# Kernel optimization log

Measured on AMD Instinct MI355X. Metric: run time of the kernel, lower is better.

The kernel has to match this reference:

```python
import jax, jax.numpy as jnp
import numpy as np

N, E, M = 100000, 1600000, 10000
D_IN, D_HID, D_OUT = 128, 128, 128


def setup_inputs() -> dict:
    key = jax.random.key(0)
    ks = jax.random.split(key, 16)
    feat = jax.random.normal(ks[0], (N, D_IN), dtype=jnp.float32)
    src = jax.random.randint(ks[1], (E,), 0, N, dtype=jnp.int32)
    dst = jax.random.randint(ks[2], (E,), 0, N, dtype=jnp.int32)
    masked_offset = jax.random.randint(ks[3], (M,), 0, N, dtype=jnp.int32)
    def xavier(k, shape):
        fan_in, fan_out = shape[0], shape[1]
        a = jnp.sqrt(6.0 / (fan_in + fan_out))
        return jax.random.uniform(k, shape, jnp.float32, -a, a)
    return {
        'feat': feat, 'src': src, 'dst': dst, 'masked_offset': masked_offset,
        # GraphConv layers (weight [in,out], bias [out])
        'W1': xavier(ks[4], (D_IN, D_HID)), 'b1': jnp.zeros((D_HID,), jnp.float32),
        'W2': xavier(ks[5], (D_HID, D_HID)), 'b2': jnp.zeros((D_HID,), jnp.float32),
        # fusion MLP
        'Wm1': xavier(ks[6], (D_HID + D_IN, D_HID)), 'bm1': jnp.zeros((D_HID,), jnp.float32),
        'Wm2': xavier(ks[7], (D_HID, D_HID)), 'bm2': jnp.zeros((D_HID,), jnp.float32),
        'Wm3': xavier(ks[8], (D_HID, D_OUT)),  # final Linear has bias=False
    }


def _graph_conv_right(h, src, dst, W, b, inv_deg):
    # DGL GraphConv(norm='right'): aggregate src features at dst, divide by in-degree.
    # Apply weight first (in_feats >= out_feats path) -- mathematically identical.
    hw = h @ W                                   # [N, out]
    agg = jax.ops.segment_sum(hw[src], dst, num_segments=N)  # scatter-add over edges
    return agg * inv_deg + b


def reference(feat, src, dst, masked_offset, W1, b1, W2, b2, Wm1, bm1, Wm2, bm2, Wm3):
    ones = jnp.ones((E,), jnp.float32)
    deg = jax.ops.segment_sum(ones, dst, num_segments=N)
    inv_deg = (1.0 / jnp.clip(deg, 1.0, None))[:, None]      # [N,1]
    # GCN layer 1 + ReLU (Identity norm)
    h = jax.nn.relu(_graph_conv_right(feat, src, dst, W1, b1, inv_deg))
    # GCN layer 2 (last layer: no activation; dropout no-op at eval)
    h = _graph_conv_right(h, src, dst, W2, b2, inv_deg)
    # fusion == 'cat': relu(Identity(h[masked])) concat raw features
    hm = jax.nn.relu(h[masked_offset])                       # [M, H]
    x = jnp.concatenate([hm, feat[masked_offset]], axis=1)   # [M, H+D]
    x = jax.nn.relu(x @ Wm1 + bm1)
    x = jax.nn.relu(x @ Wm2 + bm2)
    return x @ Wm3
```

## Files before the change

### kernel.cpp

```cpp
#include <hip/hip_runtime.h>

#define NN 100000
#define NE 1600000
#define NM 10000
#define NSB 256
#define SUBN 391
#define CAP2 7424
#define PCH 2048
#define NBP2 782
#define NBTB 1600
#define NBWC 48

typedef __attribute__((ext_vector_type(8))) short bf16x8;
typedef __attribute__((ext_vector_type(4))) float f32x4;

__device__ inline float4 ld4(const float* p) { return *(const float4*)p; }
__device__ inline float bf2f(unsigned short u) {
  union { unsigned int i; float f; } c; c.i = ((unsigned int)u) << 16; return c.f;
}
__device__ inline unsigned short f2bf(float f) {
  union { float f; unsigned int i; } c; c.f = f;
  unsigned int u = c.i + 0x7fffu + ((c.i >> 16) & 1u);
  return (unsigned short)(u >> 16);
}
__device__ inline void stx(unsigned char* base, int rowBytes, int row, int col,
                           unsigned short val) {
  int bc = col * 2;
  int c = bc >> 4, cp = c ^ (row & 15);
  *(unsigned short*)&base[row * rowBytes + (cp << 4) + (bc & 15)] = val;
}
__device__ inline bf16x8 ldx8(const unsigned char* base, int rowBytes, int row, int kc) {
  return *(const bf16x8*)&base[row * rowBytes + ((kc ^ (row & 15)) << 4)];
}

__device__ inline void convfrag(const float* W, unsigned short* Wf, int g) {
  int k8 = (g >> 7) << 3, col = g & 127;
  unsigned short tmp[8];
#pragma unroll
  for (int i = 0; i < 8; ++i) tmp[i] = f2bf(W[(k8 + i) * 128 + col]);
  *(uint4*)&Wf[(size_t)g * 8] = *(const uint4*)tmp;
}

__global__ __launch_bounds__(256) void front_k(const int* __restrict__ src,
                                               const int* __restrict__ dst,
                                               unsigned* __restrict__ parts2,
                                               int* __restrict__ pcnt2,
                                               const float* __restrict__ feat,
                                               unsigned short* __restrict__ featbf,
                                               const float* W1, const float* W2,
                                               const float* Wm1, const float* Wm2,
                                               const float* Wm3,
                                               unsigned short* W1f, unsigned short* W2f,
                                               unsigned short* Wm1f, unsigned short* Wm2f,
                                               unsigned short* Wm3f,
                                               unsigned short* __restrict__ h1bf) {
  __shared__ int cntw[4][NSB];
  __shared__ int basew[4][NSB];
  __shared__ int bstart[NSB + 1];
  __shared__ int gbase[NSB];
  __shared__ int wsum[4];
  __shared__ unsigned buf[PCH];
  __shared__ unsigned char bb[PCH];
  const int bid = blockIdx.x;
  const int tid = threadIdx.x;

  if (bid < NBP2) {
    const int wv = tid >> 6;
    const int e0 = bid * PCH;
    for (int i = tid; i < 4 * NSB; i += 256) ((int*)cntw)[i] = 0;
    __syncthreads();
    unsigned pk[8];
    int b_[8], lp_[8];
#pragma unroll
    for (int j = 0; j < 8; ++j) {
      int e = e0 + j * 256 + tid;
      bool ok = e < NE;
      int s = ok ? src[e] : 0;
      int d = ok ? dst[e] : 0;
      int b = d / SUBN;
      int ld = d - b * SUBN;
      pk[j] = ((unsigned)ld << 17) | (unsigned)s;
      b_[j] = ok ? b : -1;
      if (ok) lp_[j] = atomicAdd(&cntw[wv][b], 1);
    }
    __syncthreads();
    int t0 = cntw[0][tid], t1 = cntw[1][tid], t2 = cntw[2][tid], t3 = cntw[3][tid];
    int tot = t0 + t1 + t2 + t3;
    int x = tot;
#pragma unroll
    for (int d = 1; d < 64; d <<= 1) {
      int y = __shfl_up(x, d, 64);
      if ((tid & 63) >= d) x += y;
    }
    if ((tid & 63) == 63) wsum[wv] = x;
    __syncthreads();
    int woff = 0;
#pragma unroll
    for (int w = 0; w < 4; ++w) woff += (w < wv) ? wsum[w] : 0;
    int excl = x + woff - tot;
    bstart[tid] = excl;
    basew[0][tid] = excl;
    basew[1][tid] = excl + t0;
    basew[2][tid] = excl + t0 + t1;
    basew[3][tid] = excl + t0 + t1 + t2;
    gbase[tid] = atomicAdd(&pcnt2[tid], tot);
    if (tid == NSB - 1) bstart[NSB] = excl + tot;
    __syncthreads();
#pragma unroll
    for (int j = 0; j < 8; ++j)
      if (b_[j] >= 0) {
        int pos = basew[wv][b_[j]] + lp_[j];
        buf[pos] = pk[j];
        bb[pos] = (unsigned char)b_[j];
      }
    __syncthreads();
    int total = bstart[NSB];
    for (int i = tid; i < total; i += 256) {
      int b = bb[i];
      int gi = gbase[b] + (i - bstart[b]);
      if (gi < CAP2) parts2[(size_t)b * CAP2 + gi] = buf[i];
    }
  } else if (bid < NBP2 + NBTB) {
    const int n4 = NN * 128 / 4;
    for (int i = (bid - NBP2) * 256 + tid; i < n4; i += NBTB * 256) {
      float4 v = ld4(feat + (size_t)i * 4);
      unsigned int lo = (unsigned int)f2bf(v.x) | ((unsigned int)f2bf(v.y) << 16);
      unsigned int hi = (unsigned int)f2bf(v.z) | ((unsigned int)f2bf(v.w) << 16);
      ((uint2*)featbf)[i] = make_uint2(lo, hi);
    }
  } else if (bid < NBP2 + NBTB + NBWC) {
    int g = (bid - NBP2 - NBTB) * 256 + tid;
    if (g < 2048) convfrag(W1, W1f, g);
    else if (g < 4096) convfrag(W2, W2f, g - 2048);
    else if (g < 8192) convfrag(Wm1, Wm1f, g - 4096);
    else if (g < 10240) convfrag(Wm2, Wm2f, g - 8192);
    else if (g < 12288) convfrag(Wm3, Wm3f, g - 10240);
  } else {
    if (tid < 64) {
      ((unsigned*)(featbf + (size_t)NN * 128))[tid] = 0u;
      ((unsigned*)(h1bf + (size_t)NN * 128))[tid] = 0u;
    }
  }
}

__global__ __launch_bounds__(1024) void deg2_k(const unsigned* __restrict__ parts2,
                                               const int* __restrict__ pcnt2,
                                               int* __restrict__ deg) {
  __shared__ int cnt[SUBN];
  int sb = blockIdx.x;
  int n = min(pcnt2[sb], CAP2);
  const unsigned* p = parts2 + (size_t)sb * CAP2;
  for (int i = threadIdx.x; i < SUBN; i += 1024) cnt[i] = 0;
  __syncthreads();
  for (int i = threadIdx.x; i < n; i += 1024) atomicAdd(&cnt[p[i] >> 17], 1);
  __syncthreads();
  int base = sb * SUBN;
  for (int i = threadIdx.x; i < SUBN; i += 1024)
    if (base + i < NN) deg[base + i] = cnt[i];
}

__global__ __launch_bounds__(1024) void scan1_k(const int* __restrict__ deg,
                                                int* __restrict__ excl,
                                                int* __restrict__ bsum, int n) {
  __shared__ int lds[1024];
  int tid = threadIdx.x;
  int gid = blockIdx.x * 1024 + tid;
  int v = (gid < n) ? deg[gid] : 0;
  lds[tid] = v;
  __syncthreads();
  for (int off = 1; off < 1024; off <<= 1) {
    int t = (tid >= off) ? lds[tid - off] : 0;
    __syncthreads();
    lds[tid] += t;
    __syncthreads();
  }
  if (gid < n) excl[gid] = lds[tid] - v;
  if (tid == 1023) bsum[blockIdx.x] = lds[1023];
}

__global__ void scan2_k(int* __restrict__ bsum, int nb) {
  __shared__ int lds[128];
  int tid = threadIdx.x;
  int v = (tid < nb) ? bsum[tid] : 0;
  lds[tid] = v;
  __syncthreads();
  for (int off = 1; off < 128; off <<= 1) {
    int t = (tid >= off) ? lds[tid - off] : 0;
    __syncthreads();
    lds[tid] += t;
    __syncthreads();
  }
  if (tid < nb) bsum[tid] = lds[tid] - v;
}

__global__ __launch_bounds__(256) void scan3_k(int* __restrict__ excl,
                                               const int* __restrict__ bsum,
                                               const int* __restrict__ deg,
                                               float* __restrict__ inv, int n) {
  int gid = blockIdx.x * 256 + threadIdx.x;
  if (gid < n) {
    excl[gid] += bsum[gid >> 10] + deg[gid];
    inv[gid] = 1.0f / fmaxf((float)deg[gid], 1.0f);
  }
}

__global__ __launch_bounds__(1024) void sort_emit_k(const unsigned* __restrict__ parts2,
                                                    const int* __restrict__ pcnt2,
                                                    const int* __restrict__ offs_end,
                                                    const int* __restrict__ degv,
                                                    int* __restrict__ csr) {
  __shared__ int cur[SUBN];
  __shared__ int sorted[CAP2];
  int sb = blockIdx.x;
  int n = min(pcnt2[sb], CAP2);
  const unsigned* p = parts2 + (size_t)sb * CAP2;
  int base = sb * SUBN;
  int segbase = offs_end[base] - degv[base];
  for (int i = threadIdx.x; i < SUBN; i += 1024) {
    int nd = base + i;
    cur[i] = (nd < NN) ? (offs_end[nd] - degv[nd]) : 0;
  }
  __syncthreads();
  for (int i = threadIdx.x; i < n; i += 1024) {
    unsigned v = p[i];
    int pos = atomicAdd(&cur[v >> 17], 1);
    sorted[pos - segbase] = (int)(v & 0x1FFFFu);
  }
  __syncthreads();
  for (int i = threadIdx.x; i < n; i += 1024) csr[segbase + i] = sorted[i];
}

__global__ __launch_bounds__(256) void gather1_k(const unsigned short* __restrict__ featbf,
                                                 const int* __restrict__ csr,
                                                 const int* __restrict__ offs_end,
                                                 const int* __restrict__ degv,
                                                 const float* __restrict__ inv,
                                                 unsigned short* __restrict__ agg1) {
  int v = blockIdx.x * 8 + (threadIdx.x >> 5);
  if (v >= NN) return;
  int lane = threadIdx.x & 31;
  int cnt = degv[v];
  int start = offs_end[v] - cnt;
  const uint2* fb = (const uint2*)featbf;
  float a0 = 0.f, a1 = 0.f, a2 = 0.f, a3 = 0.f;
  int nb8 = (cnt + 7) >> 3;
  for (int it = 0; it < nb8; ++it) {
    int b = start + (it << 3);
    int rem = cnt - (it << 3);
    int sidx[8];
#pragma unroll
    for (int j = 0; j < 8; ++j) {
      int s = csr[b + (j < rem ? j : 0)];
      sidx[j] = (j < rem) ? s : NN;
    }
    uint2 x[8];
#pragma unroll
    for (int j = 0; j < 8; ++j) x[j] = fb[(size_t)sidx[j] * 32 + lane];
#pragma unroll
    for (int j = 0; j < 8; ++j) {
      a0 += bf2f((unsigned short)(x[j].x));
      a1 += bf2f((unsigned short)(x[j].x >> 16));
      a2 += bf2f((unsigned short)(x[j].y));
      a3 += bf2f((unsigned short)(x[j].y >> 16));
    }
  }
  float iv = inv[v];
  unsigned int lo = (unsigned int)f2bf(a0 * iv) | ((unsigned int)f2bf(a1 * iv) << 16);
  unsigned int hi = (unsigned int)f2bf(a2 * iv) | ((unsigned int)f2bf(a3 * iv) << 16);
  ((uint2*)agg1)[(size_t)v * 32 + lane] = make_uint2(lo, hi);
}

__global__ __launch_bounds__(256) void mfma1_k(const unsigned short* __restrict__ agg1,
                                               const unsigned short* __restrict__ W1f,
                                               const float* __restrict__ b1,
                                               unsigned short* __restrict__ h1bf) {
  const int tid = threadIdx.x;
  const int wave = tid >> 6, lane = tid & 63, l15 = lane & 15, l4 = lane >> 4;
  const int rbase = blockIdx.x * 64;
  int col0 = wave * 16 + l15, col1 = (wave + 4) * 16 + l15;
  bf16x8 Bfr0[4], Bfr1[4];
#pragma unroll
  for (int kt = 0; kt < 4; ++kt) {
    int kc = kt * 4 + l4;
    Bfr0[kt] = *(const bf16x8*)&W1f[((size_t)kc * 128 + col0) * 8];
    Bfr1[kt] = *(const bf16x8*)&W1f[((size_t)kc * 128 + col1) * 8];
  }
  float bias0 = b1[col0], bias1 = b1[col1];
  for (int rsub = 0; rsub < 4; ++rsub) {
    int arow = rbase + rsub * 16 + l15;
    const unsigned short* ap = agg1 + (size_t)min(arow, NN - 1) * 128;
    f32x4 acc0 = {0.f, 0.f, 0.f, 0.f};
    f32x4 acc1 = {0.f, 0.f, 0.f, 0.f};
#pragma unroll
    for (int kt = 0; kt < 4; ++kt) {
      int kc = kt * 4 + l4;
      bf16x8 a = *(const bf16x8*)(ap + kc * 8);
      acc0 = __builtin_amdgcn_mfma_f32_16x16x32_bf16(a, Bfr0[kt], acc0, 0, 0, 0);
      acc1 = __builtin_amdgcn_mfma_f32_16x16x32_bf16(a, Bfr1[kt], acc1, 0, 0, 0);
    }
#pragma unroll
    for (int r = 0; r < 4; ++r) {
      int orow = rbase + rsub * 16 + l4 * 4 + r;
      if (orow < NN) {
        h1bf[(size_t)orow * 128 + col0] = f2bf(fmaxf(acc0[r] + bias0, 0.f));
        h1bf[(size_t)orow * 128 + col1] = f2bf(fmaxf(acc1[r] + bias1, 0.f));
      }
    }
  }
}

__global__ __launch_bounds__(256) void gather2_k(const unsigned short* __restrict__ h1bf,
                                                 const int* __restrict__ masked,
                                                 const int* __restrict__ csr,
                                                 const int* __restrict__ offs_end,
                                                 const int* __restrict__ degv,
                                                 const float* __restrict__ inv,
                                                 unsigned short* __restrict__ agg2bf) {
  int m = blockIdx.x * 8 + (threadIdx.x >> 5);
  if (m >= NM) return;
  int lane = threadIdx.x & 31;
  int v = masked[m];
  int cnt = degv[v];
  int start = offs_end[v] - cnt;
  const uint2* fb = (const uint2*)h1bf;
  float a0 = 0.f, a1 = 0.f, a2 = 0.f, a3 = 0.f;
  int nb8 = (cnt + 7) >> 3;
  for (int it = 0; it < nb8; ++it) {
    int b = start + (it << 3);
    int rem = cnt - (it << 3);
    int sidx[8];
#pragma unroll
    for (int j = 0; j < 8; ++j) {
      int s = csr[b + (j < rem ? j : 0)];
      sidx[j] = (j < rem) ? s : NN;
    }
    uint2 x[8];
#pragma unroll
    for (int j = 0; j < 8; ++j) x[j] = fb[(size_t)sidx[j] * 32 + lane];
#pragma unroll
    for (int j = 0; j < 8; ++j) {
      a0 += bf2f((unsigned short)(x[j].x));
      a1 += bf2f((unsigned short)(x[j].x >> 16));
      a2 += bf2f((unsigned short)(x[j].y));
      a3 += bf2f((unsigned short)(x[j].y >> 16));
    }
  }
  float iv = inv[v];
  unsigned int lo = (unsigned int)f2bf(a0 * iv) | ((unsigned int)f2bf(a1 * iv) << 16);
  unsigned int hi = (unsigned int)f2bf(a2 * iv) | ((unsigned int)f2bf(a3 * iv) << 16);
  ((uint2*)agg2bf)[(size_t)m * 32 + lane] = make_uint2(lo, hi);
}

__global__ __launch_bounds__(256) void mlp_fused_k(const unsigned short* __restrict__ agg2bf,
                                                   const unsigned short* __restrict__ featbf,
                                                   const int* __restrict__ masked,
                                                   const unsigned short* __restrict__ W2f,
                                                   const float* __restrict__ b2,
                                                   const unsigned short* __restrict__ Wm1f,
                                                   const float* __restrict__ bm1,
                                                   const unsigned short* __restrict__ Wm2f,
                                                   const float* __restrict__ bm2,
                                                   const unsigned short* __restrict__ Wm3f,
                                                   float* __restrict__ out) {
  __shared__ unsigned char ldsX[64 * 512];
  __shared__ unsigned char ldsY[64 * 256];
  const int tid = threadIdx.x;
  const int rbase = blockIdx.x * 64;
  const int wave = tid >> 6, lane = tid & 63, l15 = lane & 15, l4 = lane >> 4;
  {
    int grp = tid >> 5, ln = tid & 31;
    uint2 vals[8];
#pragma unroll
    for (int k = 0; k < 8; ++k) {
      int m = rbase + grp * 8 + k;
      vals[k] = make_uint2(0u, 0u);
      if (m < NM) {
        int v = masked[m];
        vals[k] = ((const uint2*)featbf)[(size_t)v * 32 + ln];
      }
    }
#pragma unroll
    for (int k = 0; k < 8; ++k) {
      int row = grp * 8 + k;
      int c = 16 + (ln >> 1);
      *(uint2*)&ldsX[row * 512 + ((c ^ (row & 15)) << 4) + (ln & 1) * 8] = vals[k];
    }
  }
  {
    int col0 = wave * 16 + l15, col1 = (wave + 4) * 16 + l15;
    float bias0 = b2[col0], bias1 = b2[col1];
    for (int rsub = 0; rsub < 4; ++rsub) {
      int arow = rbase + rsub * 16 + l15;
      const unsigned short* ap = agg2bf + (size_t)min(arow, NM - 1) * 128;
      f32x4 acc0 = {0.f, 0.f, 0.f, 0.f};
      f32x4 acc1 = {0.f, 0.f, 0.f, 0.f};
#pragma unroll
      for (int kt = 0; kt < 4; ++kt) {
        int kc = kt * 4 + l4;
        bf16x8 a = *(const bf16x8*)(ap + kc * 8);
        bf16x8 b0 = *(const bf16x8*)&W2f[((size_t)kc * 128 + col0) * 8];
        bf16x8 b1v = *(const bf16x8*)&W2f[((size_t)kc * 128 + col1) * 8];
        acc0 = __builtin_amdgcn_mfma_f32_16x16x32_bf16(a, b0, acc0, 0, 0, 0);
        acc1 = __builtin_amdgcn_mfma_f32_16x16x32_bf16(a, b1v, acc1, 0, 0, 0);
      }
#pragma unroll
      for (int r = 0; r < 4; ++r) {
        int row = rsub * 16 + l4 * 4 + r;
        stx(ldsX, 512, row, col0, f2bf(fmaxf(acc0[r] + bias0, 0.f)));
        stx(ldsX, 512, row, col1, f2bf(fmaxf(acc1[r] + bias1, 0.f)));
      }
    }
  }
  __syncthreads();
  {
    int col0 = wave * 16 + l15, col1 = (wave + 4) * 16 + l15;
    float bias0 = bm1[col0], bias1 = bm1[col1];
    for (int rsub = 0; rsub < 4; ++rsub) {
      int row = rsub * 16 + l15;
      f32x4 acc0 = {0.f, 0.f, 0.f, 0.f};
      f32x4 acc1 = {0.f, 0.f, 0.f, 0.f};
#pragma unroll
      for (int kt = 0; kt < 8; ++kt) {
        int kc = kt * 4 + l4;
        bf16x8 a = ldx8(ldsX, 512, row, kc);
        bf16x8 b0 = *(const bf16x8*)&Wm1f[((size_t)kc * 128 + col0) * 8];
        bf16x8 b1v = *(const bf16x8*)&Wm1f[((size_t)kc * 128 + col1) * 8];
        acc0 = __builtin_amdgcn_mfma_f32_16x16x32_bf16(a, b0, acc0, 0, 0, 0);
        acc1 = __builtin_amdgcn_mfma_f32_16x16x32_bf16(a, b1v, acc1, 0, 0, 0);
      }
#pragma unroll
      for (int r = 0; r < 4; ++r) {
        int row2 = rsub * 16 + l4 * 4 + r;
        stx(ldsY, 256, row2, col0, f2bf(fmaxf(acc0[r] + bias0, 0.f)));
        stx(ldsY, 256, row2, col1, f2bf(fmaxf(acc1[r] + bias1, 0.f)));
      }
    }
  }
  __syncthreads();
  {
    int col0 = wave * 16 + l15, col1 = (wave + 4) * 16 + l15;
    float bias0 = bm2[col0], bias1 = bm2[col1];
    for (int rsub = 0; rsub < 4; ++rsub) {
      int row = rsub * 16 + l15;
      f32x4 acc0 = {0.f, 0.f, 0.f, 0.f};
      f32x4 acc1 = {0.f, 0.f, 0.f, 0.f};
#pragma unroll
      for (int kt = 0; kt < 4; ++kt) {
        int kc = kt * 4 + l4;
        bf16x8 a = ldx8(ldsY, 256, row, kc);
        bf16x8 b0 = *(const bf16x8*)&Wm2f[((size_t)kc * 128 + col0) * 8];
        bf16x8 b1v = *(const bf16x8*)&Wm2f[((size_t)kc * 128 + col1) * 8];
        acc0 = __builtin_amdgcn_mfma_f32_16x16x32_bf16(a, b0, acc0, 0, 0, 0);
        acc1 = __builtin_amdgcn_mfma_f32_16x16x32_bf16(a, b1v, acc1, 0, 0, 0);
      }
#pragma unroll
      for (int r = 0; r < 4; ++r) {
        int row2 = rsub * 16 + l4 * 4 + r;
        stx(ldsX, 256, row2, col0, f2bf(fmaxf(acc0[r] + bias0, 0.f)));
        stx(ldsX, 256, row2, col1, f2bf(fmaxf(acc1[r] + bias1, 0.f)));
      }
    }
  }
  __syncthreads();
  {
    int col0 = wave * 16 + l15, col1 = (wave + 4) * 16 + l15;
    for (int rsub = 0; rsub < 4; ++rsub) {
      int row = rsub * 16 + l15;
      f32x4 acc0 = {0.f, 0.f, 0.f, 0.f};
      f32x4 acc1 = {0.f, 0.f, 0.f, 0.f};
#pragma unroll
      for (int kt = 0; kt < 4; ++kt) {
        int kc = kt * 4 + l4;
        bf16x8 a = ldx8(ldsX, 256, row, kc);
        bf16x8 b0 = *(const bf16x8*)&Wm3f[((size_t)kc * 128 + col0) * 8];
        bf16x8 b1v = *(const bf16x8*)&Wm3f[((size_t)kc * 128 + col1) * 8];
        acc0 = __builtin_amdgcn_mfma_f32_16x16x32_bf16(a, b0, acc0, 0, 0, 0);
        acc1 = __builtin_amdgcn_mfma_f32_16x16x32_bf16(a, b1v, acc1, 0, 0, 0);
      }
#pragma unroll
      for (int r = 0; r < 4; ++r) {
        int orow = rbase + rsub * 16 + l4 * 4 + r;
        if (orow < NM) {
          out[(size_t)orow * 128 + col0] = acc0[r];
          out[(size_t)orow * 128 + col1] = acc1[r];
        }
      }
    }
  }
}

extern "C" void kernel_launch(void* const* d_in, const int* in_sizes, int n_in,
                              void* d_out, int out_size, void* d_ws, size_t ws_size,
                              hipStream_t stream) {
  const float* feat = (const float*)d_in[0];
  const int* src = (const int*)d_in[1];
  const int* dst = (const int*)d_in[2];
  const int* masked = (const int*)d_in[3];
  const float* W1 = (const float*)d_in[4];
  const float* b1 = (const float*)d_in[5];
  const float* W2 = (const float*)d_in[6];
  const float* b2 = (const float*)d_in[7];
  const float* Wm1 = (const float*)d_in[8];
  const float* bm1 = (const float*)d_in[9];
  const float* Wm2 = (const float*)d_in[10];
  const float* bm2 = (const float*)d_in[11];
  const float* Wm3 = (const float*)d_in[12];
  float* out = (float*)d_out;

  char* p = (char*)d_ws;
  int* deg = (int*)p;              p += (size_t)NN * 4;
  int* offs = (int*)p;             p += (size_t)NN * 4;
  int* bsum = (int*)p;             p += 128 * 4;
  int* pcnt2 = (int*)p;            p += NSB * 4;
  float* inv = (float*)p;          p += (size_t)NN * 4;
  int* csr = (int*)p;              p += (size_t)NE * 4;
  p = (char*)(((size_t)p + 15) & ~(size_t)15);
  unsigned* parts2 = (unsigned*)p; p += (size_t)NSB * CAP2 * 4;
  unsigned short* featbf = (unsigned short*)p;  p += (size_t)(NN + 1) * 128 * 2;
  unsigned short* agg1 = (unsigned short*)p;    p += (size_t)NN * 128 * 2;
  unsigned short* h1bf = (unsigned short*)p;    p += (size_t)(NN + 1) * 128 * 2;
  unsigned short* agg2bf = (unsigned short*)p;  p += (size_t)NM * 128 * 2;
  unsigned short* W1f = (unsigned short*)p;     p += 16384 * 2;
  unsigned short* W2f = (unsigned short*)p;     p += 16384 * 2;
  unsigned short* Wm1f = (unsigned short*)p;    p += 32768 * 2;
  unsigned short* Wm2f = (unsigned short*)p;    p += 16384 * 2;
  unsigned short* Wm3f = (unsigned short*)p;    p += 16384 * 2;

  (void)hipMemsetAsync(pcnt2, 0, NSB * 4, stream);

  front_k<<<NBP2 + NBTB + NBWC + 1, 256, 0, stream>>>(
      src, dst, parts2, pcnt2, feat, featbf,
      W1, W2, Wm1, Wm2, Wm3, W1f, W2f, Wm1f, Wm2f, Wm3f, h1bf);

  deg2_k<<<NSB, 1024, 0, stream>>>(parts2, pcnt2, deg);
  int nb = (NN + 1023) / 1024;
  scan1_k<<<nb, 1024, 0, stream>>>(deg, offs, bsum, NN);
  scan2_k<<<1, 128, 0, stream>>>(bsum, nb);
  scan3_k<<<(NN + 255) / 256, 256, 0, stream>>>(offs, bsum, deg, inv, NN);
  sort_emit_k<<<NSB, 1024, 0, stream>>>(parts2, pcnt2, offs, deg, csr);

  gather1_k<<<(NN + 7) / 8, 256, 0, stream>>>(featbf, csr, offs, deg, inv, agg1);
  mfma1_k<<<(NN + 63) / 64, 256, 0, stream>>>(agg1, W1f, b1, h1bf);

  gather2_k<<<(NM + 7) / 8, 256, 0, stream>>>(h1bf, masked, csr, offs, deg, inv, agg2bf);

  mlp_fused_k<<<(NM + 63) / 64, 256, 0, stream>>>(agg2bf, featbf, masked,
                                                  W2f, b2, Wm1f, bm1, Wm2f, bm2, Wm3f, out);
}
```

Measured before the change: 158.6 us.

## Fuse degree count, scans and CSR emission into one build kernel; pack bf16 unpack

Replaces five kernels (degree count, three-pass global scan, sort/emit) with a single per-bucket kernel. Each block computes its global base by scanning the bucket counts in shared memory and does a local scan of node degrees, which removes four launches and the global round trips. Each block now repeats a small 256-entry scan of pcnt2. The gather kernels also switch the bf16 unpack to shift/mask into float2 accumulators so packed adds may be used.

After: 152.5 us. 1.04x faster.

```diff
diff --git a/kernel.cpp b/kernel.cpp
--- a/kernel.cpp
+++ b/kernel.cpp
@@ -13,6 +13,7 @@
 
 typedef __attribute__((ext_vector_type(8))) short bf16x8;
 typedef __attribute__((ext_vector_type(4))) float f32x4;
+typedef __attribute__((ext_vector_type(2))) float f32x2;
 
 __device__ inline float4 ld4(const float* p) { return *(const float4*)p; }
 __device__ inline float bf2f(unsigned short u) {
@@ -143,91 +144,62 @@
   }
 }
 
-__global__ __launch_bounds__(1024) void deg2_k(const unsigned* __restrict__ parts2,
-                                               const int* __restrict__ pcnt2,
-                                               int* __restrict__ deg) {
+__global__ __launch_bounds__(1024) void build_k(const unsigned* __restrict__ parts2,
+                                                const int* __restrict__ pcnt2,
+                                                int* __restrict__ deg,
+                                                int* __restrict__ offs_end,
+                                                float* __restrict__ inv,
+                                                int* __restrict__ csr) {
   __shared__ int cnt[SUBN];
-  int sb = blockIdx.x;
-  int n = min(pcnt2[sb], CAP2);
+  __shared__ int scn[512];
+  __shared__ int cur[SUBN];
+  __shared__ int sbb[NSB];
+  __shared__ int sorted[CAP2];
+  const int sb = blockIdx.x;
+  const int tid = threadIdx.x;
+  const int n = min(pcnt2[sb], CAP2);
   const unsigned* p = parts2 + (size_t)sb * CAP2;
-  for (int i = threadIdx.x; i < SUBN; i += 1024) cnt[i] = 0;
-  __syncthreads();
-  for (int i = threadIdx.x; i < n; i += 1024) atomicAdd(&cnt[p[i] >> 17], 1);
-  __syncthreads();
-  int base = sb * SUBN;
-  for (int i = threadIdx.x; i < SUBN; i += 1024)
-    if (base + i < NN) deg[base + i] = cnt[i];
-}
-
-__global__ __launch_bounds__(1024) void scan1_k(const int* __restrict__ deg,
-                                                int* __restrict__ excl,
-                                                int* __restrict__ bsum, int n) {
-  __shared__ int lds[1024];
-  int tid = threadIdx.x;
-  int gid = blockIdx.x * 1024 + tid;
-  int v = (gid < n) ? deg[gid] : 0;
-  lds[tid] = v;
-  __syncthreads();
-  for (int off = 1; off < 1024; off <<= 1) {
-    int t = (tid >= off) ? lds[tid - off] : 0;
-    __syncthreads();
-    lds[tid] += t;
-    __syncthreads();
-  }
-  if (gid < n) excl[gid] = lds[tid] - v;
-  if (tid == 1023) bsum[blockIdx.x] = lds[1023];
-}
-
-__global__ void scan2_k(int* __restrict__ bsum, int nb) {
-  __shared__ int lds[128];
-  int tid = threadIdx.x;
-  int v = (tid < nb) ? bsum[tid] : 0;
-  lds[tid] = v;
-  __syncthreads();
-  for (int off = 1; off < 128; off <<= 1) {
-    int t = (tid >= off) ? lds[tid - off] : 0;
-    __syncthreads();
-    lds[tid] += t;
-    __syncthreads();
-  }
-  if (tid < nb) bsum[tid] = lds[tid] - v;
-}
-
-__global__ __launch_bounds__(256) void scan3_k(int* __restrict__ excl,
-                                               const int* __restrict__ bsum,
-                                               const int* __restrict__ deg,
-                                               float* __restrict__ inv, int n) {
-  int gid = blockIdx.x * 256 + threadIdx.x;
-  if (gid < n) {
-    excl[gid] += bsum[gid >> 10] + deg[gid];
-    inv[gid] = 1.0f / fmaxf((float)deg[gid], 1.0f);
-  }
-}
-
-__global__ __launch_bounds__(1024) void sort_emit_k(const unsigned* __restrict__ parts2,
-                                                    const int* __restrict__ pcnt2,
-                                                    const int* __restrict__ offs_end,
-                                                    const int* __restrict__ degv,
-                                                    int* __restrict__ csr) {
-  __shared__ int cur[SUBN];
-  __shared__ int sorted[CAP2];
-  int sb = blockIdx.x;
-  int n = min(pcnt2[sb], CAP2);
-  const unsigned* p = parts2 + (size_t)sb * CAP2;
-  int base = sb * SUBN;
-  int segbase = offs_end[base] - degv[base];
-  for (int i = threadIdx.x; i < SUBN; i += 1024) {
+
+  if (tid < NSB) sbb[tid] = min(pcnt2[tid], CAP2);
+  for (int i = tid; i < SUBN; i += 1024) cnt[i] = 0;
+  __syncthreads();
+  for (int off = 1; off < NSB; off <<= 1) {
+    int t = (tid >= off && tid < NSB) ? sbb[tid - off] : 0;
+    __syncthreads();
+    if (tid < NSB) sbb[tid] += t;
+    __syncthreads();
+  }
+  for (int i = tid; i < n; i += 1024) atomicAdd(&cnt[p[i] >> 17], 1);
+  __syncthreads();
+  if (tid < 512) scn[tid] = (tid < SUBN) ? cnt[tid] : 0;
+  __syncthreads();
+  for (int off = 1; off < 512; off <<= 1) {
+    int t = (tid >= off && tid < 512) ? scn[tid - off] : 0;
+    __syncthreads();
+    if (tid < 512) scn[tid] += t;
+    __syncthreads();
+  }
+  const int segbase = (sb == 0) ? 0 : sbb[sb - 1];
+  const int base = sb * SUBN;
+  for (int i = tid; i < SUBN; i += 1024) {
+    int c = cnt[i];
+    int loff = scn[i] - c;
+    cur[i] = loff;
     int nd = base + i;
-    cur[i] = (nd < NN) ? (offs_end[nd] - degv[nd]) : 0;
-  }
-  __syncthreads();
-  for (int i = threadIdx.x; i < n; i += 1024) {
+    if (nd < NN) {
+      deg[nd] = c;
+      offs_end[nd] = segbase + loff + c;
+      inv[nd] = 1.0f / fmaxf((float)c, 1.0f);
+    }
+  }
+  __syncthreads();
+  for (int i = tid; i < n; i += 1024) {
     unsigned v = p[i];
     int pos = atomicAdd(&cur[v >> 17], 1);
-    sorted[pos - segbase] = (int)(v & 0x1FFFFu);
-  }
-  __syncthreads();
-  for (int i = threadIdx.x; i < n; i += 1024) csr[segbase + i] = sorted[i];
+    sorted[pos] = (int)(v & 0x1FFFFu);
+  }
+  __syncthreads();
+  for (int i = tid; i < n; i += 1024) csr[segbase + i] = sorted[i];
 }
 
 __global__ __launch_bounds__(256) void gather1_k(const unsigned short* __restrict__ featbf,
@@ -242,7 +214,7 @@
   int cnt = degv[v];
   int start = offs_end[v] - cnt;
   const uint2* fb = (const uint2*)featbf;
-  float a0 = 0.f, a1 = 0.f, a2 = 0.f, a3 = 0.f;
+  f32x2 a01 = {0.f, 0.f}, a23 = {0.f, 0.f};
   int nb8 = (cnt + 7) >> 3;
   for (int it = 0; it < nb8; ++it) {
     int b = start + (it << 3);
@@ -258,15 +230,18 @@
     for (int j = 0; j < 8; ++j) x[j] = fb[(size_t)sidx[j] * 32 + lane];
 #pragma unroll
     for (int j = 0; j < 8; ++j) {
-      a0 += bf2f((unsigned short)(x[j].x));
-      a1 += bf2f((unsigned short)(x[j].x >> 16));
-      a2 += bf2f((unsigned short)(x[j].y));
-      a3 += bf2f((unsigned short)(x[j].y >> 16));
+      f32x2 u, w;
+      u.x = __uint_as_float(x[j].x << 16);
+      u.y = __uint_as_float(x[j].x & 0xFFFF0000u);
+      w.x = __uint_as_float(x[j].y << 16);
+      w.y = __uint_as_float(x[j].y & 0xFFFF0000u);
+      a01 += u;
+      a23 += w;
     }
   }
   float iv = inv[v];
-  unsigned int lo = (unsigned int)f2bf(a0 * iv) | ((unsigned int)f2bf(a1 * iv) << 16);
-  unsigned int hi = (unsigned int)f2bf(a2 * iv) | ((unsigned int)f2bf(a3 * iv) << 16);
+  unsigned int lo = (unsigned int)f2bf(a01.x * iv) | ((unsigned int)f2bf(a01.y * iv) << 16);
+  unsigned int hi = (unsigned int)f2bf(a23.x * iv) | ((unsigned int)f2bf(a23.y * iv) << 16);
   ((uint2*)agg1)[(size_t)v * 32 + lane] = make_uint2(lo, hi);
 }
 
@@ -323,7 +298,7 @@
   int cnt = degv[v];
   int start = offs_end[v] - cnt;
   const uint2* fb = (const uint2*)h1bf;
-  float a0 = 0.f, a1 = 0.f, a2 = 0.f, a3 = 0.f;
+  f32x2 a01 = {0.f, 0.f}, a23 = {0.f, 0.f};
   int nb8 = (cnt + 7) >> 3;
   for (int it = 0; it < nb8; ++it) {
     int b = start + (it << 3);
@@ -339,15 +314,18 @@
     for (int j = 0; j < 8; ++j) x[j] = fb[(size_t)sidx[j] * 32 + lane];
 #pragma unroll
     for (int j = 0; j < 8; ++j) {
-      a0 += bf2f((unsigned short)(x[j].x));
-      a1 += bf2f((unsigned short)(x[j].x >> 16));
-      a2 += bf2f((unsigned short)(x[j].y));
-      a3 += bf2f((unsigned short)(x[j].y >> 16));
+      f32x2 u, w;
+      u.x = __uint_as_float(x[j].x << 16);
+      u.y = __uint_as_float(x[j].x & 0xFFFF0000u);
+      w.x = __uint_as_float(x[j].y << 16);
+      w.y = __uint_as_float(x[j].y & 0xFFFF0000u);
+      a01 += u;
+      a23 += w;
     }
   }
   float iv = inv[v];
-  unsigned int lo = (unsigned int)f2bf(a0 * iv) | ((unsigned int)f2bf(a1 * iv) << 16);
-  unsigned int hi = (unsigned int)f2bf(a2 * iv) | ((unsigned int)f2bf(a3 * iv) << 16);
+  unsigned int lo = (unsigned int)f2bf(a01.x * iv) | ((unsigned int)f2bf(a01.y * iv) << 16);
+  unsigned int hi = (unsigned int)f2bf(a23.x * iv) | ((unsigned int)f2bf(a23.y * iv) << 16);
   ((uint2*)agg2bf)[(size_t)m * 32 + lane] = make_uint2(lo, hi);
 }
 
@@ -510,7 +488,6 @@
   char* p = (char*)d_ws;
   int* deg = (int*)p;              p += (size_t)NN * 4;
   int* offs = (int*)p;             p += (size_t)NN * 4;
-  int* bsum = (int*)p;             p += 128 * 4;
   int* pcnt2 = (int*)p;            p += NSB * 4;
   float* inv = (float*)p;          p += (size_t)NN * 4;
   int* csr = (int*)p;              p += (size_t)NE * 4;
@@ -532,12 +509,7 @@
       src, dst, parts2, pcnt2, feat, featbf,
       W1, W2, Wm1, Wm2, Wm3, W1f, W2f, Wm1f, Wm2f, Wm3f, h1bf);
 
-  deg2_k<<<NSB, 1024, 0, stream>>>(parts2, pcnt2, deg);
-  int nb = (NN + 1023) / 1024;
-  scan1_k<<<nb, 1024, 0, stream>>>(deg, offs, bsum, NN);
-  scan2_k<<<1, 128, 0, stream>>>(bsum, nb);
-  scan3_k<<<(NN + 255) / 256, 256, 0, stream>>>(offs, bsum, deg, inv, NN);
-  sort_emit_k<<<NSB, 1024, 0, stream>>>(parts2, pcnt2, offs, deg, csr);
+  build_k<<<NSB, 1024, 0, stream>>>(parts2, pcnt2, deg, offs, inv, csr);
 
   gather1_k<<<(NN + 7) / 8, 256, 0, stream>>>(featbf, csr, offs, deg, inv, agg1);
   mfma1_k<<<(NN + 63) / 64, 256, 0, stream>>>(agg1, W1f, b1, h1bf);
```
